# Optimization experiments

Measured on AMD Instinct MI355X. Metric: run time of the kernel, lower is better.

The kernel has to match this reference:

```python
import jax, jax.numpy as jnp
import numpy as np

NEG_SLOPE = 0.2
EPS = 1e-16


def _gat_conv(x, src, dst, edge_attr, W, We, att_src, att_dst, att_edge, bias):
    """PyG GATConv, heads=H, concat=False, edge_dim given. x:[N,F_in]."""
    N = x.shape[0]
    H, C = att_src.shape
    xs = (x @ W.T).reshape(N, H, C)                      # [N,H,C]
    a_src = jnp.einsum('nhc,hc->nh', xs, att_src)        # [N,H]
    a_dst = jnp.einsum('nhc,hc->nh', xs, att_dst)        # [N,H]
    e = (edge_attr @ We.T).reshape(-1, H, C)             # [E,H,C]
    a_edge = jnp.einsum('ehc,hc->eh', e, att_edge)       # [E,H]
    alpha = a_src[src] + a_dst[dst] + a_edge             # [E,H]
    alpha = jax.nn.leaky_relu(alpha, NEG_SLOPE)
    # segment softmax over destination nodes (per head)
    amax = jax.ops.segment_max(alpha, dst, num_segments=N)   # [N,H]
    ex = jnp.exp(alpha - amax[dst])
    denom = jax.ops.segment_sum(ex, dst, num_segments=N)     # [N,H]
    alpha = ex / (denom[dst] + EPS)
    msg = xs[src] * alpha[..., None]                     # [E,H,C]
    out = jax.ops.segment_sum(msg, dst, num_segments=N)  # [N,H,C]
    return out.mean(axis=1) + bias                       # concat=False -> mean over heads


def _add_self_loops(src, dst, edge_attr, N):
    # PyG add_self_loops with fill_value='mean': per-dst mean of incoming edge_attr
    ones = jnp.ones((edge_attr.shape[0],), edge_attr.dtype)
    sums = jax.ops.segment_sum(edge_attr, dst, num_segments=N)
    cnt = jax.ops.segment_sum(ones, dst, num_segments=N)
    loop_attr = sums / jnp.maximum(cnt, 1.0)[:, None]
    idx = jnp.arange(N, dtype=src.dtype)
    return (jnp.concatenate([src, idx]), jnp.concatenate([dst, idx]),
            jnp.concatenate([edge_attr, loop_attr], axis=0))


def setup_inputs() -> dict:
    key = jax.random.key(0)
    ks = jax.random.split(key, 16)
    N, E, F_IN, C, H = 100000, 1600000, 64, 32, 4
    s = 0.1
    inp = {
        'x': jax.random.normal(ks[0], (N, F_IN), jnp.float32),
        'edge_index': jax.random.randint(ks[1], (2, E), 0, N, jnp.int32),
        'edge_weight': jax.random.uniform(ks[2], (E, 1), jnp.float32),
        'w1': jax.random.normal(ks[3], (H * C, F_IN), jnp.float32) * s,
        'we1': jax.random.normal(ks[4], (H * C, 1), jnp.float32) * s,
        'as1': jax.random.normal(ks[5], (H, C), jnp.float32) * s,
        'ad1': jax.random.normal(ks[6], (H, C), jnp.float32) * s,
        'ae1': jax.random.normal(ks[7], (H, C), jnp.float32) * s,
        'b1': jnp.zeros((C,), jnp.float32),
        'w2': jax.random.normal(ks[8], (H * C, C), jnp.float32) * s,
        'we2': jax.random.normal(ks[9], (H * C, 1), jnp.float32) * s,
        'as2': jax.random.normal(ks[10], (H, C), jnp.float32) * s,
        'ad2': jax.random.normal(ks[11], (H, C), jnp.float32) * s,
        'ae2': jax.random.normal(ks[12], (H, C), jnp.float32) * s,
        'b2': jnp.zeros((C,), jnp.float32),
    }
    return inp


def reference(x, edge_index, edge_weight, w1, we1, as1, ad1, ae1, b1,
              w2, we2, as2, ad2, ae2, b2):
    N = x.shape[0]
    src, dst, ea = _add_self_loops(edge_index[0], edge_index[1], edge_weight, N)
    h = jax.nn.relu(_gat_conv(x, src, dst, ea, w1, we1, as1, ad1, ae1, b1))
    # nn.Dropout is identity in eval mode
    h = jax.nn.relu(_gat_conv(h, src, dst, ea, w2, we2, as2, ad2, ae2, b2))
    return h
```

## Files before the change

kernel.cpp:

```cpp
#include <hip/hip_runtime.h>
#include <hip/hip_fp16.h>
#include <cstddef>

#define GAT_EPS 1e-16f
#define CAP 48

__global__ __launch_bounds__(256, 2)
void k_gemm1h(const float* __restrict__ x, const float* __restrict__ W,
              const float* __restrict__ as_, const float* __restrict__ ad_,
              __half* __restrict__ xs, float* __restrict__ asrc,
              float* __restrict__ adst, int N, int gemmb,
              const int* __restrict__ src, const int* __restrict__ dst,
              const float* __restrict__ ew, int* __restrict__ cnt,
              int2* __restrict__ epk, int E,
              const float* __restrict__ we1, const float* __restrict__ ae1,
              const float* __restrict__ we2, const float* __restrict__ ae2,
              float* __restrict__ wd,
              const float* __restrict__ as2, const float* __restrict__ ad2,
              const float* __restrict__ W2, float* __restrict__ vs2,
              float* __restrict__ vd2) {
    if (blockIdx.x == gridDim.x - 1) {
        int t = threadIdx.x;
        if (t < 128) {
            float v1 = we1[t] * ae1[t];
            float v2 = we2[t] * ae2[t];
#pragma unroll
            for (int off = 16; off; off >>= 1) {
                v1 += __shfl_xor(v1, off);
                v2 += __shfl_xor(v2, off);
            }
            if ((t & 31) == 0) { wd[t >> 5] = v1; wd[4 + (t >> 5)] = v2; }
            int h = t >> 5, c = t & 31;
            float s = 0.f, dv = 0.f;
            for (int k = 0; k < 32; k++) {
                float w = W2[(h * 32 + k) * 32 + c];
                s  += as2[h * 32 + k] * w;
                dv += ad2[h * 32 + k] * w;
            }
            vs2[t] = s;
            vd2[t] = dv;
        }
        return;
    }
    int g = blockIdx.x / 5;
    int r = blockIdx.x % 5;
    if (r != 0) {
        int i = (g * 4 + r - 1) * 256 + threadIdx.x;
        if (i < E) {
            int d = dst[i];
            int p = atomicAdd(&cnt[d], 1);
            p = min(p, CAP - 1);
            int2 q; q.x = src[i]; q.y = __float_as_int(ew[i]);
            epk[(size_t)d * CAP + p] = q;
        }
        return;
    }
    if (g >= gemmb) return;

    int n0 = g * 64;
    int t = threadIdx.x;
    int tx = t & 31;
    int ty = t >> 5;
    __shared__ __half Wh[64 * 132];
    __shared__ float xsh[64 * 65];
    int nrows = min(64, N - n0);
    for (int j = t; j < 8192; j += 256) {
        int c = j >> 6, k = j & 63;
        Wh[k * 132 + ((c & 31) << 2) + (c >> 5)] = __float2half(W[j]);
    }
    const float* xg = x + (size_t)n0 * 64;
    for (int j = t; j < nrows * 64; j += 256) xsh[(j >> 6) * 65 + (j & 63)] = xg[j];
    __syncthreads();

    float acc[8][4];
#pragma unroll
    for (int i = 0; i < 8; i++)
#pragma unroll
        for (int j = 0; j < 4; j++) acc[i][j] = 0.f;

#pragma unroll 4
    for (int k = 0; k < 64; k++) {
        const __half2* wp = reinterpret_cast<const __half2*>(&Wh[k * 132 + (tx << 2)]);
        float2 wf0 = __half22float2(wp[0]);
        float2 wf1 = __half22float2(wp[1]);
#pragma unroll
        for (int i = 0; i < 8; i++) {
            float xv = xsh[(ty * 8 + i) * 65 + k];
            acc[i][0] += xv * wf0.x;
            acc[i][1] += xv * wf0.y;
            acc[i][2] += xv * wf1.x;
            acc[i][3] += xv * wf1.y;
        }
    }

    float asv[4], adv[4];
#pragma unroll
    for (int j = 0; j < 4; j++) { asv[j] = as_[32 * j + tx]; adv[j] = ad_[32 * j + tx]; }

#pragma unroll
    for (int i = 0; i < 8; i++) {
        int row = ty * 8 + i;
        bool ok = row < nrows;
        __half* orow = xs + (size_t)(n0 + row) * 128;
#pragma unroll
        for (int j = 0; j < 4; j++) {
            if (ok) orow[32 * j + tx] = __float2half(acc[i][j]);
            float vs = acc[i][j] * asv[j];
            float vd = acc[i][j] * adv[j];
#pragma unroll
            for (int off = 16; off; off >>= 1) {
                vs += __shfl_xor(vs, off);
                vd += __shfl_xor(vd, off);
            }
            if (ok && tx == 0) {
                asrc[(size_t)(n0 + row) * 4 + j] = vs;
                adst[(size_t)(n0 + row) * 4 + j] = vd;
            }
        }
    }
}

__global__ void k_gather1(const int2* __restrict__ epk, const int* __restrict__ cnt,
                          const __half* __restrict__ xs,
                          const float* __restrict__ asrc, const float* __restrict__ adst,
                          const float* __restrict__ wedot, const float* __restrict__ bias,
                          const float* __restrict__ vs2, const float* __restrict__ vd2,
                          __half2* __restrict__ h1, float* __restrict__ asrc2,
                          float* __restrict__ adst2, int N) {
    int node = blockIdx.x * 4 + (threadIdx.x >> 6);
    if (node >= N) return;
    int l = threadIdx.x & 63;
    int q = l >> 4;
    int p = l & 15;
    int h = p >> 2;
    float wd = wedot[h];
    float ad = adst[(size_t)node * 4 + h];
    int cv = min(cnt[node], CAP);
    int beg = node * CAP;
    int end = beg + cv;

    float a0 = 0.f, a1 = 0.f, a2 = 0.f, a3 = 0.f;
    float a4 = 0.f, a5 = 0.f, a6 = 0.f, a7 = 0.f, ds = 0.f, easum = 0.f;
#pragma unroll 2
    for (int i = beg; i < end; i += 4) {
        int idx = i + q;
        bool valid = idx < end;
        int2 e = epk[valid ? idx : end - 1];
        int s = e.x;
        float eav = valid ? __int_as_float(e.y) : 0.f;
        easum += eav;
        float as = asrc[(size_t)s * 4 + h];
        float al = as + ad + __int_as_float(e.y) * wd;
        al = fmaxf(al, 0.2f * al);
        float w = valid ? __expf(al) : 0.f;
        uint4 raw = reinterpret_cast<const uint4*>(xs + (size_t)s * 128)[p];
        const __half2* hp = reinterpret_cast<const __half2*>(&raw);
        float2 f0 = __half22float2(hp[0]);
        float2 f1 = __half22float2(hp[1]);
        float2 f2 = __half22float2(hp[2]);
        float2 f3 = __half22float2(hp[3]);
        a0 += w * f0.x; a1 += w * f0.y;
        a2 += w * f1.x; a3 += w * f1.y;
        a4 += w * f2.x; a5 += w * f2.y;
        a6 += w * f3.x; a7 += w * f3.y;
        ds += w;
    }
    easum += __shfl_xor(easum, 16);
    easum += __shfl_xor(easum, 32);
    float loop_ea = easum / fmaxf((float)cv, 1.0f);
    float aln = asrc[(size_t)node * 4 + h] + ad + loop_ea * wd;
    aln = fmaxf(aln, 0.2f * aln);
    float wl = __expf(aln);
    if (q == 0) {
        uint4 raw = reinterpret_cast<const uint4*>(xs + (size_t)node * 128)[p];
        const __half2* hp = reinterpret_cast<const __half2*>(&raw);
        float2 f0 = __half22float2(hp[0]);
        float2 f1 = __half22float2(hp[1]);
        float2 f2 = __half22float2(hp[2]);
        float2 f3 = __half22float2(hp[3]);
        a0 += wl * f0.x; a1 += wl * f0.y;
        a2 += wl * f1.x; a3 += wl * f1.y;
        a4 += wl * f2.x; a5 += wl * f2.y;
        a6 += wl * f3.x; a7 += wl * f3.y;
        ds += wl;
    }
    a0 += __shfl_xor(a0, 16); a1 += __shfl_xor(a1, 16);
    a2 += __shfl_xor(a2, 16); a3 += __shfl_xor(a3, 16);
    a4 += __shfl_xor(a4, 16); a5 += __shfl_xor(a5, 16);
    a6 += __shfl_xor(a6, 16); a7 += __shfl_xor(a7, 16);
    ds += __shfl_xor(ds, 16);
    a0 += __shfl_xor(a0, 32); a1 += __shfl_xor(a1, 32);
    a2 += __shfl_xor(a2, 32); a3 += __shfl_xor(a3, 32);
    a4 += __shfl_xor(a4, 32); a5 += __shfl_xor(a5, 32);
    a6 += __shfl_xor(a6, 32); a7 += __shfl_xor(a7, 32);
    ds += __shfl_xor(ds, 32);
    float inv = 1.f / (ds + GAT_EPS);
    a0 *= inv; a1 *= inv; a2 *= inv; a3 *= inv;
    a4 *= inv; a5 *= inv; a6 *= inv; a7 *= inv;
    a0 += __shfl_xor(a0, 4); a1 += __shfl_xor(a1, 4);
    a2 += __shfl_xor(a2, 4); a3 += __shfl_xor(a3, 4);
    a4 += __shfl_xor(a4, 4); a5 += __shfl_xor(a5, 4);
    a6 += __shfl_xor(a6, 4); a7 += __shfl_xor(a7, 4);
    a0 += __shfl_xor(a0, 8); a1 += __shfl_xor(a1, 8);
    a2 += __shfl_xor(a2, 8); a3 += __shfl_xor(a3, 8);
    a4 += __shfl_xor(a4, 8); a5 += __shfl_xor(a5, 8);
    a6 += __shfl_xor(a6, 8); a7 += __shfl_xor(a7, 8);
    if (l < 4) {
        int c0 = l * 8;
        float rv[8];
        rv[0] = fmaxf(0.25f * a0 + bias[c0 + 0], 0.f);
        rv[1] = fmaxf(0.25f * a1 + bias[c0 + 1], 0.f);
        rv[2] = fmaxf(0.25f * a2 + bias[c0 + 2], 0.f);
        rv[3] = fmaxf(0.25f * a3 + bias[c0 + 3], 0.f);
        rv[4] = fmaxf(0.25f * a4 + bias[c0 + 4], 0.f);
        rv[5] = fmaxf(0.25f * a5 + bias[c0 + 5], 0.f);
        rv[6] = fmaxf(0.25f * a6 + bias[c0 + 6], 0.f);
        rv[7] = fmaxf(0.25f * a7 + bias[c0 + 7], 0.f);
        __half2* hp = h1 + (size_t)node * 16 + l * 4;
        hp[0] = __floats2half2_rn(rv[0], rv[1]);
        hp[1] = __floats2half2_rn(rv[2], rv[3]);
        hp[2] = __floats2half2_rn(rv[4], rv[5]);
        hp[3] = __floats2half2_rn(rv[6], rv[7]);
        float pa[4] = {0.f, 0.f, 0.f, 0.f}, pd[4] = {0.f, 0.f, 0.f, 0.f};
#pragma unroll
        for (int hh = 0; hh < 4; hh++)
#pragma unroll
            for (int j = 0; j < 8; j++) {
                pa[hh] += rv[j] * vs2[hh * 32 + c0 + j];
                pd[hh] += rv[j] * vd2[hh * 32 + c0 + j];
            }
#pragma unroll
        for (int hh = 0; hh < 4; hh++) {
            pa[hh] += __shfl_xor(pa[hh], 1);
            pa[hh] += __shfl_xor(pa[hh], 2);
            pd[hh] += __shfl_xor(pd[hh], 1);
            pd[hh] += __shfl_xor(pd[hh], 2);
        }
        if (l == 0) {
            float4 wa, wb;
            wa.x = pa[0]; wa.y = pa[1]; wa.z = pa[2]; wa.w = pa[3];
            wb.x = pd[0]; wb.y = pd[1]; wb.z = pd[2]; wb.w = pd[3];
            *reinterpret_cast<float4*>(asrc2 + (size_t)node * 4) = wa;
            *reinterpret_cast<float4*>(adst2 + (size_t)node * 4) = wb;
        }
    }
}

__global__ void k_gather2(const int2* __restrict__ epk, const int* __restrict__ cnt,
                          const __half* __restrict__ h1,
                          const float* __restrict__ asrc, const float* __restrict__ adst,
                          const float* __restrict__ wedot, const float* __restrict__ W2,
                          const float* __restrict__ bias, float* __restrict__ out, int N) {
    __shared__ float W2sh[128 * 33];
    __shared__ float Ash[4][128];
    int t = threadIdx.x;
    for (int j = t; j < 4096; j += 256) {
        int hh = j >> 10, k = (j >> 5) & 31, c = j & 31;
        W2sh[(hh * 32 + c) * 33 + k] = W2[j];
    }
    __syncthreads();

    int node0 = blockIdx.x * 4 + (t >> 6);
    bool live = node0 < N;
    int node = live ? node0 : 0;
    int l = t & 63;
    int q = l >> 4;
    int g = l & 15;
    int h = g >> 2;
    int j4 = g & 3;
    float wd = wedot[h];
    float ad = adst[(size_t)node * 4 + h];
    int cv = min(cnt[node], CAP);
    int beg = node * CAP;
    int end = beg + cv;

    float A0 = 0.f, A1 = 0.f, A2 = 0.f, A3 = 0.f;
    float A4 = 0.f, A5 = 0.f, A6 = 0.f, A7 = 0.f;
    float ds = 0.f, easum = 0.f;
#pragma unroll 2
    for (int i = beg; i < end; i += 4) {
        int idx = i + q;
        bool valid = idx < end;
        int2 e = epk[valid ? idx : end - 1];
        int s = e.x;
        float eav = valid ? __int_as_float(e.y) : 0.f;
        easum += eav;
        float as = asrc[(size_t)s * 4 + h];
        float al = as + ad + __int_as_float(e.y) * wd;
        al = fmaxf(al, 0.2f * al);
        float w = valid ? __expf(al) : 0.f;
        uint4 raw = reinterpret_cast<const uint4*>(h1 + (size_t)s * 32)[j4];
        const __half2* hp = reinterpret_cast<const __half2*>(&raw);
        float2 f0 = __half22float2(hp[0]);
        float2 f1 = __half22float2(hp[1]);
        float2 f2 = __half22float2(hp[2]);
        float2 f3 = __half22float2(hp[3]);
        A0 += w * f0.x; A1 += w * f0.y;
        A2 += w * f1.x; A3 += w * f1.y;
        A4 += w * f2.x; A5 += w * f2.y;
        A6 += w * f3.x; A7 += w * f3.y;
        ds += w;
    }
    easum += __shfl_xor(easum, 16);
    easum += __shfl_xor(easum, 32);
    float loop_ea = easum / fmaxf((float)cv, 1.0f);
    float aln = asrc[(size_t)node * 4 + h] + ad + loop_ea * wd;
    aln = fmaxf(aln, 0.2f * aln);
    float wl = __expf(aln);
    if (q == 0) {
        uint4 raw = reinterpret_cast<const uint4*>(h1 + (size_t)node * 32)[j4];
        const __half2* hp = reinterpret_cast<const __half2*>(&raw);
        float2 f0 = __half22float2(hp[0]);
        float2 f1 = __half22float2(hp[1]);
        float2 f2 = __half22float2(hp[2]);
        float2 f3 = __half22float2(hp[3]);
        A0 += wl * f0.x; A1 += wl * f0.y;
        A2 += wl * f1.x; A3 += wl * f1.y;
        A4 += wl * f2.x; A5 += wl * f2.y;
        A6 += wl * f3.x; A7 += wl * f3.y;
        ds += wl;
    }
    A0 += __shfl_xor(A0, 16); A1 += __shfl_xor(A1, 16);
    A2 += __shfl_xor(A2, 16); A3 += __shfl_xor(A3, 16);
    A4 += __shfl_xor(A4, 16); A5 += __shfl_xor(A5, 16);
    A6 += __shfl_xor(A6, 16); A7 += __shfl_xor(A7, 16);
    ds += __shfl_xor(ds, 16);
    A0 += __shfl_xor(A0, 32); A1 += __shfl_xor(A1, 32);
    A2 += __shfl_xor(A2, 32); A3 += __shfl_xor(A3, 32);
    A4 += __shfl_xor(A4, 32); A5 += __shfl_xor(A5, 32);
    A6 += __shfl_xor(A6, 32); A7 += __shfl_xor(A7, 32);
    ds += __shfl_xor(ds, 32);
    float inv = 1.f / (ds + GAT_EPS);
    if (q == 0) {
        float* ap = &Ash[t >> 6][h * 32 + j4 * 8];
        ap[0] = A0 * inv; ap[1] = A1 * inv; ap[2] = A2 * inv; ap[3] = A3 * inv;
        ap[4] = A4 * inv; ap[5] = A5 * inv; ap[6] = A6 * inv; ap[7] = A7 * inv;
    }
    __syncthreads();
    int k = l & 31;
    int hp2 = l >> 5;
    const float* arow = Ash[t >> 6];
    float part = 0.f;
#pragma unroll
    for (int hh = 2 * hp2; hh <= 2 * hp2 + 1; hh++) {
        const float* wrow = &W2sh[(hh * 32) * 33 + k];
#pragma unroll 8
        for (int c = 0; c < 32; c++)
            part += arow[hh * 32 + c] * wrow[c * 33];
    }
    part += __shfl_xor(part, 32);
    if (live && l < 32)
        out[(size_t)node * 32 + k] = fmaxf(0.25f * part + bias[k], 0.f);
}

extern "C" void kernel_launch(void* const* d_in, const int* in_sizes, int n_in,
                              void* d_out, int out_size, void* d_ws, size_t ws_size,
                              hipStream_t stream) {
    const float* x   = (const float*)d_in[0];
    const int*   ei  = (const int*)d_in[1];
    const float* ewt = (const float*)d_in[2];
    const float* w1  = (const float*)d_in[3];
    const float* we1 = (const float*)d_in[4];
    const float* as1 = (const float*)d_in[5];
    const float* ad1 = (const float*)d_in[6];
    const float* ae1 = (const float*)d_in[7];
    const float* b1  = (const float*)d_in[8];
    const float* w2  = (const float*)d_in[9];
    const float* we2 = (const float*)d_in[10];
    const float* as2 = (const float*)d_in[11];
    const float* ad2 = (const float*)d_in[12];
    const float* ae2 = (const float*)d_in[13];
    const float* b2  = (const float*)d_in[14];

    const int N = in_sizes[0] / 64;
    const int E = in_sizes[1] / 2;
    const int* srcI = ei;
    const int* dstI = ei + E;

    char* base = (char*)d_ws;
    size_t off = 0;
    auto alloc = [&](size_t bytes) { char* p = base + off; off += (bytes + 15) & ~(size_t)15; return p; };
    __half* xs     = (__half*)alloc((size_t)N * 128 * sizeof(__half));
    __half2* h1    = (__half2*)alloc((size_t)N * 16 * sizeof(__half2));
    float* asrc    = (float*)alloc((size_t)N * 4 * sizeof(float));
    float* adst    = (float*)alloc((size_t)N * 4 * sizeof(float));
    float* asrc2   = (float*)alloc((size_t)N * 4 * sizeof(float));
    float* adst2   = (float*)alloc((size_t)N * 4 * sizeof(float));
    int*   cnt     = (int*)alloc((size_t)N * sizeof(int));
    int2*  epk     = (int2*)alloc((size_t)N * CAP * sizeof(int2));
    float* wedot   = (float*)alloc(8 * sizeof(float));
    float* vs2     = (float*)alloc(128 * sizeof(float));
    float* vd2     = (float*)alloc(128 * sizeof(float));

    float* outF = (float*)d_out;

    hipMemsetAsync(cnt, 0, (size_t)N * sizeof(int), stream);

    const int gemmb = (N + 63) / 64;
    const int histb = (E + 255) / 256;
    const int G = gemmb > (histb + 3) / 4 ? gemmb : (histb + 3) / 4;
    const int gb = (N + 3) / 4;

    k_gemm1h<<<5 * G + 1, 256, 0, stream>>>(x, w1, as1, ad1, xs, asrc, adst, N, gemmb,
                                            srcI, dstI, ewt, cnt, epk, E,
                                            we1, ae1, we2, ae2, wedot,
                                            as2, ad2, w2, vs2, vd2);

    k_gather1<<<gb, 256, 0, stream>>>(epk, cnt, xs, asrc, adst,
                                      wedot + 0, b1, vs2, vd2, h1, asrc2, adst2, N);

    k_gather2<<<gb, 256, 0, stream>>>(epk, cnt, (const __half*)h1, asrc2, adst2,
                                      wedot + 4, w2, b2, outF, N);
}
```

Before: 321.5 us.

## Aggregate raw x before layer-1 projection, applying W1 after gather

Layer 1 now gathers the 64-wide half-precision input rows instead of the 128-wide projected features. Each destination keeps one weighted sum of x per head and multiplies it by W1 after aggregation, which is valid because the projection is linear. The attention logits come from precomputed vectors W1^T·att, so the dense GEMM in the prep kernel becomes a cheap per-node dot product. This halves gather bytes per edge but doubles per-edge accumulators (two heads per lane) and adds a block-level shared-memory matmul and a __syncthreads in the gather kernel.

Measured after the change: 422.2 us. +31.3%, slower.

```diff
diff --git a/kernel.cpp b/kernel.cpp
--- a/kernel.cpp
+++ b/kernel.cpp
@@ -6,21 +6,26 @@
 #define CAP 48
 
 __global__ __launch_bounds__(256, 2)
-void k_gemm1h(const float* __restrict__ x, const float* __restrict__ W,
-              const float* __restrict__ as_, const float* __restrict__ ad_,
-              __half* __restrict__ xs, float* __restrict__ asrc,
-              float* __restrict__ adst, int N, int gemmb,
-              const int* __restrict__ src, const int* __restrict__ dst,
-              const float* __restrict__ ew, int* __restrict__ cnt,
-              int2* __restrict__ epk, int E,
-              const float* __restrict__ we1, const float* __restrict__ ae1,
-              const float* __restrict__ we2, const float* __restrict__ ae2,
-              float* __restrict__ wd,
-              const float* __restrict__ as2, const float* __restrict__ ad2,
-              const float* __restrict__ W2, float* __restrict__ vs2,
-              float* __restrict__ vd2) {
+void k_prep(const float* __restrict__ x, const float* __restrict__ W1,
+            const float* __restrict__ as1, const float* __restrict__ ad1,
+            __half* __restrict__ xh, float* __restrict__ asrc,
+            float* __restrict__ adst, int N,
+            const int* __restrict__ src, const int* __restrict__ dst,
+            const float* __restrict__ ew, int* __restrict__ cnt,
+            int2* __restrict__ epk, int E,
+            const float* __restrict__ we1, const float* __restrict__ ae1,
+            const float* __restrict__ we2, const float* __restrict__ ae2,
+            float* __restrict__ wd,
+            const float* __restrict__ as2, const float* __restrict__ ad2,
+            const float* __restrict__ W2, float* __restrict__ vs2,
+            float* __restrict__ vd2, __half2* __restrict__ w1h) {
+    int t = threadIdx.x;
     if (blockIdx.x == gridDim.x - 1) {
-        int t = threadIdx.x;
+        for (int j = t; j < 4096; j += 256) {
+            int k = j >> 6, cp = j & 63;
+            w1h[k * 64 + cp] = __floats2half2_rn(W1[(2 * cp) * 64 + k],
+                                                 (float)W1[(2 * cp + 1) * 64 + k]);
+        }
         if (t < 128) {
             float v1 = we1[t] * ae1[t];
             float v2 = we2[t] * ae2[t];
@@ -45,7 +50,7 @@
     int g = blockIdx.x / 5;
     int r = blockIdx.x % 5;
     if (r != 0) {
-        int i = (g * 4 + r - 1) * 256 + threadIdx.x;
+        int i = (g * 4 + r - 1) * 256 + t;
         if (i < E) {
             int d = dst[i];
             int p = atomicAdd(&cnt[d], 1);
@@ -55,194 +60,179 @@
         }
         return;
     }
-    if (g >= gemmb) return;
-
+    __shared__ float vs1sh[4][64], vd1sh[4][64];
+    {
+        int h = t >> 6, k = t & 63;
+        float s = 0.f, dv = 0.f;
+        for (int c = 0; c < 32; c++) {
+            float w = W1[(h * 32 + c) * 64 + k];
+            s  += as1[h * 32 + c] * w;
+            dv += ad1[h * 32 + c] * w;
+        }
+        vs1sh[h][k] = s;
+        vd1sh[h][k] = dv;
+    }
+    __syncthreads();
     int n0 = g * 64;
-    int t = threadIdx.x;
-    int tx = t & 31;
-    int ty = t >> 5;
-    __shared__ __half Wh[64 * 132];
-    __shared__ float xsh[64 * 65];
-    int nrows = min(64, N - n0);
-    for (int j = t; j < 8192; j += 256) {
-        int c = j >> 6, k = j & 63;
-        Wh[k * 132 + ((c & 31) << 2) + (c >> 5)] = __float2half(W[j]);
-    }
-    const float* xg = x + (size_t)n0 * 64;
-    for (int j = t; j < nrows * 64; j += 256) xsh[(j >> 6) * 65 + (j & 63)] = xg[j];
-    __syncthreads();
-
-    float acc[8][4];
-#pragma unroll
-    for (int i = 0; i < 8; i++)
-#pragma unroll
-        for (int j = 0; j < 4; j++) acc[i][j] = 0.f;
-
-#pragma unroll 4
-    for (int k = 0; k < 64; k++) {
-        const __half2* wp = reinterpret_cast<const __half2*>(&Wh[k * 132 + (tx << 2)]);
-        float2 wf0 = __half22float2(wp[0]);
-        float2 wf1 = __half22float2(wp[1]);
-#pragma unroll
-        for (int i = 0; i < 8; i++) {
-            float xv = xsh[(ty * 8 + i) * 65 + k];
-            acc[i][0] += xv * wf0.x;
-            acc[i][1] += xv * wf0.y;
-            acc[i][2] += xv * wf1.x;
-            acc[i][3] += xv * wf1.y;
-        }
-    }
-
-    float asv[4], adv[4];
-#pragma unroll
-    for (int j = 0; j < 4; j++) { asv[j] = as_[32 * j + tx]; adv[j] = ad_[32 * j + tx]; }
-
-#pragma unroll
-    for (int i = 0; i < 8; i++) {
-        int row = ty * 8 + i;
-        bool ok = row < nrows;
-        __half* orow = xs + (size_t)(n0 + row) * 128;
-#pragma unroll
-        for (int j = 0; j < 4; j++) {
-            if (ok) orow[32 * j + tx] = __float2half(acc[i][j]);
-            float vs = acc[i][j] * asv[j];
-            float vd = acc[i][j] * adv[j];
-#pragma unroll
-            for (int off = 16; off; off >>= 1) {
-                vs += __shfl_xor(vs, off);
-                vd += __shfl_xor(vd, off);
-            }
-            if (ok && tx == 0) {
-                asrc[(size_t)(n0 + row) * 4 + j] = vs;
-                adst[(size_t)(n0 + row) * 4 + j] = vd;
-            }
+    int wv = t >> 6, lane = t & 63;
+    for (int it = 0; it < 16; it++) {
+        int node = n0 + it * 4 + wv;
+        if (node >= N) break;
+        float xv = x[(size_t)node * 64 + lane];
+        xh[(size_t)node * 64 + lane] = __float2half(xv);
+        float p0 = xv * vs1sh[0][lane], p1 = xv * vs1sh[1][lane];
+        float p2 = xv * vs1sh[2][lane], p3 = xv * vs1sh[3][lane];
+        float q0 = xv * vd1sh[0][lane], q1 = xv * vd1sh[1][lane];
+        float q2 = xv * vd1sh[2][lane], q3 = xv * vd1sh[3][lane];
+#pragma unroll
+        for (int off = 32; off; off >>= 1) {
+            p0 += __shfl_xor(p0, off); p1 += __shfl_xor(p1, off);
+            p2 += __shfl_xor(p2, off); p3 += __shfl_xor(p3, off);
+            q0 += __shfl_xor(q0, off); q1 += __shfl_xor(q1, off);
+            q2 += __shfl_xor(q2, off); q3 += __shfl_xor(q3, off);
+        }
+        if (lane == 0) {
+            float4 a; a.x = p0; a.y = p1; a.z = p2; a.w = p3;
+            float4 b; b.x = q0; b.y = q1; b.z = q2; b.w = q3;
+            *reinterpret_cast<float4*>(asrc + (size_t)node * 4) = a;
+            *reinterpret_cast<float4*>(adst + (size_t)node * 4) = b;
         }
     }
 }
 
 __global__ void k_gather1(const int2* __restrict__ epk, const int* __restrict__ cnt,
-                          const __half* __restrict__ xs,
+                          const __half* __restrict__ xh, const __half2* __restrict__ w1h,
                           const float* __restrict__ asrc, const float* __restrict__ adst,
                           const float* __restrict__ wedot, const float* __restrict__ bias,
                           const float* __restrict__ vs2, const float* __restrict__ vd2,
                           __half2* __restrict__ h1, float* __restrict__ asrc2,
                           float* __restrict__ adst2, int N) {
-    int node = blockIdx.x * 4 + (threadIdx.x >> 6);
-    if (node >= N) return;
-    int l = threadIdx.x & 63;
+    __shared__ __half2 W1sh[64 * 67];
+    __shared__ float Ash[4][4][64];
+    int t = threadIdx.x;
+    for (int j = t; j < 4096; j += 256)
+        W1sh[(j >> 6) * 67 + (j & 63)] = w1h[j];
+    __syncthreads();
+
+    int node0 = blockIdx.x * 4 + (t >> 6);
+    bool live = node0 < N;
+    int node = live ? node0 : 0;
+    int wv = t >> 6;
+    int l = t & 63;
     int q = l >> 4;
-    int p = l & 15;
-    int h = p >> 2;
-    float wd = wedot[h];
-    float ad = adst[(size_t)node * 4 + h];
+    int rh = (l >> 3) & 1;
+    int p = l & 7;
+    float wd0 = wedot[2 * rh], wd1 = wedot[2 * rh + 1];
+    float2 adv = *reinterpret_cast<const float2*>(adst + (size_t)node * 4 + 2 * rh);
     int cv = min(cnt[node], CAP);
-    int beg = node * CAP;
-    int end = beg + cv;
-
-    float a0 = 0.f, a1 = 0.f, a2 = 0.f, a3 = 0.f;
-    float a4 = 0.f, a5 = 0.f, a6 = 0.f, a7 = 0.f, ds = 0.f, easum = 0.f;
-#pragma unroll 2
+    int beg = node * CAP, end = beg + cv;
+
+    float A0[8] = {0.f, 0.f, 0.f, 0.f, 0.f, 0.f, 0.f, 0.f};
+    float A1[8] = {0.f, 0.f, 0.f, 0.f, 0.f, 0.f, 0.f, 0.f};
+    float ds0 = 0.f, ds1 = 0.f, easum = 0.f;
     for (int i = beg; i < end; i += 4) {
         int idx = i + q;
         bool valid = idx < end;
         int2 e = epk[valid ? idx : end - 1];
         int s = e.x;
-        float eav = valid ? __int_as_float(e.y) : 0.f;
-        easum += eav;
-        float as = asrc[(size_t)s * 4 + h];
-        float al = as + ad + __int_as_float(e.y) * wd;
-        al = fmaxf(al, 0.2f * al);
-        float w = valid ? __expf(al) : 0.f;
-        uint4 raw = reinterpret_cast<const uint4*>(xs + (size_t)s * 128)[p];
+        float ea = __int_as_float(e.y);
+        easum += valid ? ea : 0.f;
+        float2 asv = *reinterpret_cast<const float2*>(asrc + (size_t)s * 4 + 2 * rh);
+        float al0 = asv.x + adv.x + ea * wd0; al0 = fmaxf(al0, 0.2f * al0);
+        float al1 = asv.y + adv.y + ea * wd1; al1 = fmaxf(al1, 0.2f * al1);
+        float w0 = valid ? __expf(al0) : 0.f;
+        float w1v = valid ? __expf(al1) : 0.f;
+        uint4 raw = reinterpret_cast<const uint4*>(xh + (size_t)s * 64)[p];
         const __half2* hp = reinterpret_cast<const __half2*>(&raw);
-        float2 f0 = __half22float2(hp[0]);
-        float2 f1 = __half22float2(hp[1]);
-        float2 f2 = __half22float2(hp[2]);
-        float2 f3 = __half22float2(hp[3]);
-        a0 += w * f0.x; a1 += w * f0.y;
-        a2 += w * f1.x; a3 += w * f1.y;
-        a4 += w * f2.x; a5 += w * f2.y;
-        a6 += w * f3.x; a7 += w * f3.y;
-        ds += w;
+#pragma unroll
+        for (int jj = 0; jj < 4; jj++) {
+            float2 f = __half22float2(hp[jj]);
+            A0[2 * jj]     += w0 * f.x;  A0[2 * jj + 1] += w0 * f.y;
+            A1[2 * jj]     += w1v * f.x; A1[2 * jj + 1] += w1v * f.y;
+        }
+        ds0 += w0; ds1 += w1v;
     }
     easum += __shfl_xor(easum, 16);
     easum += __shfl_xor(easum, 32);
     float loop_ea = easum / fmaxf((float)cv, 1.0f);
-    float aln = asrc[(size_t)node * 4 + h] + ad + loop_ea * wd;
-    aln = fmaxf(aln, 0.2f * aln);
-    float wl = __expf(aln);
+    float2 asn = *reinterpret_cast<const float2*>(asrc + (size_t)node * 4 + 2 * rh);
+    float aln0 = asn.x + adv.x + loop_ea * wd0; aln0 = fmaxf(aln0, 0.2f * aln0);
+    float aln1 = asn.y + adv.y + loop_ea * wd1; aln1 = fmaxf(aln1, 0.2f * aln1);
+    float wl0 = __expf(aln0), wl1 = __expf(aln1);
     if (q == 0) {
-        uint4 raw = reinterpret_cast<const uint4*>(xs + (size_t)node * 128)[p];
+        uint4 raw = reinterpret_cast<const uint4*>(xh + (size_t)node * 64)[p];
         const __half2* hp = reinterpret_cast<const __half2*>(&raw);
-        float2 f0 = __half22float2(hp[0]);
-        float2 f1 = __half22float2(hp[1]);
-        float2 f2 = __half22float2(hp[2]);
-        float2 f3 = __half22float2(hp[3]);
-        a0 += wl * f0.x; a1 += wl * f0.y;
-        a2 += wl * f1.x; a3 += wl * f1.y;
-        a4 += wl * f2.x; a5 += wl * f2.y;
-        a6 += wl * f3.x; a7 += wl * f3.y;
-        ds += wl;
-    }
-    a0 += __shfl_xor(a0, 16); a1 += __shfl_xor(a1, 16);
-    a2 += __shfl_xor(a2, 16); a3 += __shfl_xor(a3, 16);
-    a4 += __shfl_xor(a4, 16); a5 += __shfl_xor(a5, 16);
-    a6 += __shfl_xor(a6, 16); a7 += __shfl_xor(a7, 16);
-    ds += __shfl_xor(ds, 16);
-    a0 += __shfl_xor(a0, 32); a1 += __shfl_xor(a1, 32);
-    a2 += __shfl_xor(a2, 32); a3 += __shfl_xor(a3, 32);
-    a4 += __shfl_xor(a4, 32); a5 += __shfl_xor(a5, 32);
-    a6 += __shfl_xor(a6, 32); a7 += __shfl_xor(a7, 32);
-    ds += __shfl_xor(ds, 32);
-    float inv = 1.f / (ds + GAT_EPS);
-    a0 *= inv; a1 *= inv; a2 *= inv; a3 *= inv;
-    a4 *= inv; a5 *= inv; a6 *= inv; a7 *= inv;
-    a0 += __shfl_xor(a0, 4); a1 += __shfl_xor(a1, 4);
-    a2 += __shfl_xor(a2, 4); a3 += __shfl_xor(a3, 4);
-    a4 += __shfl_xor(a4, 4); a5 += __shfl_xor(a5, 4);
-    a6 += __shfl_xor(a6, 4); a7 += __shfl_xor(a7, 4);
-    a0 += __shfl_xor(a0, 8); a1 += __shfl_xor(a1, 8);
-    a2 += __shfl_xor(a2, 8); a3 += __shfl_xor(a3, 8);
-    a4 += __shfl_xor(a4, 8); a5 += __shfl_xor(a5, 8);
-    a6 += __shfl_xor(a6, 8); a7 += __shfl_xor(a7, 8);
-    if (l < 4) {
-        int c0 = l * 8;
-        float rv[8];
-        rv[0] = fmaxf(0.25f * a0 + bias[c0 + 0], 0.f);
-        rv[1] = fmaxf(0.25f * a1 + bias[c0 + 1], 0.f);
-        rv[2] = fmaxf(0.25f * a2 + bias[c0 + 2], 0.f);
-        rv[3] = fmaxf(0.25f * a3 + bias[c0 + 3], 0.f);
-        rv[4] = fmaxf(0.25f * a4 + bias[c0 + 4], 0.f);
-        rv[5] = fmaxf(0.25f * a5 + bias[c0 + 5], 0.f);
-        rv[6] = fmaxf(0.25f * a6 + bias[c0 + 6], 0.f);
-        rv[7] = fmaxf(0.25f * a7 + bias[c0 + 7], 0.f);
-        __half2* hp = h1 + (size_t)node * 16 + l * 4;
-        hp[0] = __floats2half2_rn(rv[0], rv[1]);
-        hp[1] = __floats2half2_rn(rv[2], rv[3]);
-        hp[2] = __floats2half2_rn(rv[4], rv[5]);
-        hp[3] = __floats2half2_rn(rv[6], rv[7]);
-        float pa[4] = {0.f, 0.f, 0.f, 0.f}, pd[4] = {0.f, 0.f, 0.f, 0.f};
-#pragma unroll
-        for (int hh = 0; hh < 4; hh++)
-#pragma unroll
-            for (int j = 0; j < 8; j++) {
-                pa[hh] += rv[j] * vs2[hh * 32 + c0 + j];
-                pd[hh] += rv[j] * vd2[hh * 32 + c0 + j];
-            }
-#pragma unroll
-        for (int hh = 0; hh < 4; hh++) {
-            pa[hh] += __shfl_xor(pa[hh], 1);
-            pa[hh] += __shfl_xor(pa[hh], 2);
-            pd[hh] += __shfl_xor(pd[hh], 1);
-            pd[hh] += __shfl_xor(pd[hh], 2);
-        }
-        if (l == 0) {
-            float4 wa, wb;
-            wa.x = pa[0]; wa.y = pa[1]; wa.z = pa[2]; wa.w = pa[3];
-            wb.x = pd[0]; wb.y = pd[1]; wb.z = pd[2]; wb.w = pd[3];
-            *reinterpret_cast<float4*>(asrc2 + (size_t)node * 4) = wa;
-            *reinterpret_cast<float4*>(adst2 + (size_t)node * 4) = wb;
-        }
+#pragma unroll
+        for (int jj = 0; jj < 4; jj++) {
+            float2 f = __half22float2(hp[jj]);
+            A0[2 * jj]     += wl0 * f.x; A0[2 * jj + 1] += wl0 * f.y;
+            A1[2 * jj]     += wl1 * f.x; A1[2 * jj + 1] += wl1 * f.y;
+        }
+        ds0 += wl0; ds1 += wl1;
+    }
+#pragma unroll
+    for (int jj = 0; jj < 8; jj++) {
+        A0[jj] += __shfl_xor(A0[jj], 16); A0[jj] += __shfl_xor(A0[jj], 32);
+        A1[jj] += __shfl_xor(A1[jj], 16); A1[jj] += __shfl_xor(A1[jj], 32);
+    }
+    ds0 += __shfl_xor(ds0, 16); ds0 += __shfl_xor(ds0, 32);
+    ds1 += __shfl_xor(ds1, 16); ds1 += __shfl_xor(ds1, 32);
+    float inv0 = 1.f / (ds0 + GAT_EPS);
+    float inv1 = 1.f / (ds1 + GAT_EPS);
+    if (q == 0) {
+        float4* a0p = reinterpret_cast<float4*>(&Ash[wv][2 * rh][p * 8]);
+        float4 v;
+        v.x = A0[0] * inv0; v.y = A0[1] * inv0; v.z = A0[2] * inv0; v.w = A0[3] * inv0;
+        a0p[0] = v;
+        v.x = A0[4] * inv0; v.y = A0[5] * inv0; v.z = A0[6] * inv0; v.w = A0[7] * inv0;
+        a0p[1] = v;
+        float4* a1p = reinterpret_cast<float4*>(&Ash[wv][2 * rh + 1][p * 8]);
+        v.x = A1[0] * inv1; v.y = A1[1] * inv1; v.z = A1[2] * inv1; v.w = A1[3] * inv1;
+        a1p[0] = v;
+        v.x = A1[4] * inv1; v.y = A1[5] * inv1; v.z = A1[6] * inv1; v.w = A1[7] * inv1;
+        a1p[1] = v;
+    }
+    __syncthreads();
+    int c2 = l & 15, qtr = l >> 4;
+    const float* arow = &Ash[wv][0][0];
+    float ac0 = 0.f, ac1 = 0.f;
+#pragma unroll
+    for (int hh = 0; hh < 4; hh++) {
+#pragma unroll
+        for (int kk = 0; kk < 16; kk++) {
+            int k = qtr * 16 + kk;
+            float av = arow[hh * 64 + k];
+            float2 wv2 = __half22float2(W1sh[k * 67 + hh * 16 + c2]);
+            ac0 += av * wv2.x;
+            ac1 += av * wv2.y;
+        }
+    }
+    ac0 += __shfl_xor(ac0, 16); ac0 += __shfl_xor(ac0, 32);
+    ac1 += __shfl_xor(ac1, 16); ac1 += __shfl_xor(ac1, 32);
+    float r0 = fmaxf(0.25f * ac0 + bias[2 * c2], 0.f);
+    float r1 = fmaxf(0.25f * ac1 + bias[2 * c2 + 1], 0.f);
+    if (live && l < 16)
+        h1[(size_t)node * 16 + c2] = __floats2half2_rn(r0, r1);
+    float pa0 = r0 * vs2[2 * c2]      + r1 * vs2[2 * c2 + 1];
+    float pa1 = r0 * vs2[32 + 2 * c2] + r1 * vs2[32 + 2 * c2 + 1];
+    float pa2 = r0 * vs2[64 + 2 * c2] + r1 * vs2[64 + 2 * c2 + 1];
+    float pa3 = r0 * vs2[96 + 2 * c2] + r1 * vs2[96 + 2 * c2 + 1];
+    float pd0 = r0 * vd2[2 * c2]      + r1 * vd2[2 * c2 + 1];
+    float pd1 = r0 * vd2[32 + 2 * c2] + r1 * vd2[32 + 2 * c2 + 1];
+    float pd2 = r0 * vd2[64 + 2 * c2] + r1 * vd2[64 + 2 * c2 + 1];
+    float pd3 = r0 * vd2[96 + 2 * c2] + r1 * vd2[96 + 2 * c2 + 1];
+#pragma unroll
+    for (int off = 1; off < 16; off <<= 1) {
+        pa0 += __shfl_xor(pa0, off); pa1 += __shfl_xor(pa1, off);
+        pa2 += __shfl_xor(pa2, off); pa3 += __shfl_xor(pa3, off);
+        pd0 += __shfl_xor(pd0, off); pd1 += __shfl_xor(pd1, off);
+        pd2 += __shfl_xor(pd2, off); pd3 += __shfl_xor(pd3, off);
+    }
+    if (live && l == 0) {
+        float4 a; a.x = pa0; a.y = pa1; a.z = pa2; a.w = pa3;
+        float4 b; b.x = pd0; b.y = pd1; b.z = pd2; b.w = pd3;
+        *reinterpret_cast<float4*>(asrc2 + (size_t)node * 4) = a;
+        *reinterpret_cast<float4*>(adst2 + (size_t)node * 4) = b;
     }
 }
 
@@ -380,7 +370,7 @@
     char* base = (char*)d_ws;
     size_t off = 0;
     auto alloc = [&](size_t bytes) { char* p = base + off; off += (bytes + 15) & ~(size_t)15; return p; };
-    __half* xs     = (__half*)alloc((size_t)N * 128 * sizeof(__half));
+    __half* xh     = (__half*)alloc((size_t)N * 64 * sizeof(__half));
     __half2* h1    = (__half2*)alloc((size_t)N * 16 * sizeof(__half2));
     float* asrc    = (float*)alloc((size_t)N * 4 * sizeof(float));
     float* adst    = (float*)alloc((size_t)N * 4 * sizeof(float));
@@ -391,22 +381,23 @@
     float* wedot   = (float*)alloc(8 * sizeof(float));
     float* vs2     = (float*)alloc(128 * sizeof(float));
     float* vd2     = (float*)alloc(128 * sizeof(float));
+    __half2* w1h   = (__half2*)alloc(4096 * sizeof(__half2));
 
     float* outF = (float*)d_out;
 
     hipMemsetAsync(cnt, 0, (size_t)N * sizeof(int), stream);
 
-    const int gemmb = (N + 63) / 64;
+    const int convb = (N + 63) / 64;
     const int histb = (E + 255) / 256;
-    const int G = gemmb > (histb + 3) / 4 ? gemmb : (histb + 3) / 4;
+    const int G = convb > (histb + 3) / 4 ? convb : (histb + 3) / 4;
     const int gb = (N + 3) / 4;
 
-    k_gemm1h<<<5 * G + 1, 256, 0, stream>>>(x, w1, as1, ad1, xs, asrc, adst, N, gemmb,
-                                            srcI, dstI, ewt, cnt, epk, E,
-                                            we1, ae1, we2, ae2, wedot,
-                                            as2, ad2, w2, vs2, vd2);
-
-    k_gather1<<<gb, 256, 0, stream>>>(epk, cnt, xs, asrc, adst,
+    k_prep<<<5 * G + 1, 256, 0, stream>>>(x, w1, as1, ad1, xh, asrc, adst, N,
+                                          srcI, dstI, ewt, cnt, epk, E,
+                                          we1, ae1, we2, ae2, wedot,
+                                          as2, ad2, w2, vs2, vd2, w1h);
+
+    k_gather1<<<gb, 256, 0, stream>>>(epk, cnt, xh, w1h, asrc, adst,
                                       wedot + 0, b1, vs2, vd2, h1, asrc2, adst2, N);
 
     k_gather2<<<gb, 256, 0, stream>>>(epk, cnt, (const __half*)h1, asrc2, adst2,
```
